# Optimization experiments

Measured on AMD Instinct MI355X. Metric: run time of the kernel, lower is better.

The kernel has to match this reference:

```python
import jax, jax.numpy as jnp
import numpy as np

B, S, D, H = 4, 2048, 1024, 16
NEG = -1e10  # matches the module's -10000000000.0 additive mask


def setup_inputs() -> dict:
    key = jax.random.key(0)
    k1, k2, k3, k4, k5 = jax.random.split(key, 5)
    scale = 0.02
    return {
        "x": jax.random.normal(k1, (B, S, D), dtype=jnp.float32),
        "w_qkv": jax.random.normal(k2, (D, 3 * D), dtype=jnp.float32) * scale,
        "b_qkv": jax.random.normal(k3, (3 * D,), dtype=jnp.float32) * scale,
        "w_out": jax.random.normal(k4, (D, D), dtype=jnp.float32) * scale,
        "b_out": jax.random.normal(k5, (D,), dtype=jnp.float32) * scale,
    }


def reference(x, w_qkv, b_qkv, w_out, b_out):
    b, s, d = x.shape
    hd = d // H  # per-head dim
    qkv = x @ w_qkv + b_qkv  # [b,s,3d]
    qq, kk, vv = jnp.split(qkv, 3, axis=-1)
    # [b,h,s,hd]
    qq = qq.reshape(b, s, H, hd).transpose(0, 2, 1, 3)
    kk = kk.reshape(b, s, H, hd).transpose(0, 2, 1, 3)
    vv = vv.reshape(b, s, H, hd).transpose(0, 2, 1, 3)
    scale = 1.0 / float(hd) ** 0.5
    # additive causal mask: NEG above diagonal, 0 on/below (as in module)
    mask = (1.0 - jnp.tri(s, dtype=jnp.float32)) * NEG
    attn = jnp.einsum("bhqd,bhkd->bhqk", qq, kk) * scale + mask
    attn = jax.nn.softmax(attn, axis=-1)
    out = jnp.einsum("bhqk,bhkd->bhqd", attn, vv)  # [b,h,s,hd]
    out = out.transpose(0, 2, 1, 3).reshape(b, s, d)
    return out @ w_out + b_out
```

## Files before the change

kernel.cpp:

```cpp
#include <hip/hip_runtime.h>
#include <hip/hip_bf16.h>
#include <stdint.h>


#define B_   4
#define S_   2048
#define D_   1024
#define H_   16
#define HD_  64
#define MTOK (B_ * S_)
#define BK   32
#define QSCALE 0.18033688011112042f

typedef __attribute__((ext_vector_type(8))) short bfx8;
typedef __attribute__((ext_vector_type(4))) float fx4;

static __device__ __forceinline__ unsigned short f2bf(float f) {
    union { float f; uint32_t u; } v{f};
    uint32_t u = v.u;
    u += 0x7fffu + ((u >> 16) & 1u);
    return (unsigned short)(u >> 16);
}

static __device__ __forceinline__ uint32_t cvtpk(float lo, float hi) {
    uint32_t r;
    asm volatile("v_cvt_pk_bf16_f32 %0, %1, %2" : "=v"(r) : "v"(lo), "v"(hi));
    return r;
}

static __device__ __forceinline__ void gll16(const unsigned short* g, const unsigned short* l) {
    typedef const __attribute__((address_space(1))) void* gp_t;
    typedef __attribute__((address_space(3))) void* lp_t;
    __builtin_amdgcn_global_load_lds((gp_t)(uintptr_t)g, (lp_t)(uint32_t)(uintptr_t)l, 16, 0, 0);
}

__global__ void k_conv_x(const float* __restrict__ x, unsigned short* __restrict__ xb, int n8) {
    int i = blockIdx.x * blockDim.x + threadIdx.x;
    int stride = gridDim.x * blockDim.x;
    for (; i < n8; i += stride) {
        const float4* p = (const float4*)(x + (size_t)i * 8);
        float4 a = p[0], b = p[1];
        bfx8 o;
        o[0]=f2bf(a.x); o[1]=f2bf(a.y); o[2]=f2bf(a.z); o[3]=f2bf(a.w);
        o[4]=f2bf(b.x); o[5]=f2bf(b.y); o[6]=f2bf(b.z); o[7]=f2bf(b.w);
        *(bfx8*)(xb + (size_t)i * 8) = o;
    }
}

__global__ void k_transpose_bf(const float* __restrict__ w, unsigned short* __restrict__ wt,
                               int K, int N) {
    int idx = blockIdx.x * blockDim.x + threadIdx.x;
    int total = N * (K / 8);
    if (idx >= total) return;
    int n  = idx % N;
    int k0 = (idx / N) * 8;
    bfx8 o;
#pragma unroll
    for (int j = 0; j < 8; ++j) o[j] = f2bf(w[(size_t)(k0 + j) * N + n]);
    *(bfx8*)(wt + (size_t)n * K + k0) = o;
}

__global__ void k_transpose_v(const unsigned short* __restrict__ Vw,
                              unsigned short* __restrict__ Vt) {
    __shared__ unsigned short lds[64][72];
    const int bg = blockIdx.x;
    const int bh = bg >> 5;
    const int st = (bg & 31) * 64;
    const int t = threadIdx.x;
#pragma unroll
    for (int j = 0; j < 2; ++j) {
        int c = t + 256 * j;
        int row = c >> 3, q = c & 7;
        *(bfx8*)&lds[row][q * 8] = *(const bfx8*)&Vw[((size_t)bh * S_ + st + row) * HD_ + q * 8];
    }
    __syncthreads();
#pragma unroll
    for (int j = 0; j < 2; ++j) {
        int c = t + 256 * j;
        int d = c >> 3, q = c & 7;
        bfx8 o;
#pragma unroll
        for (int e = 0; e < 8; ++e) o[e] = lds[q * 8 + e][d];
        *(bfx8*)&Vt[((size_t)bh * HD_ + d) * S_ + st + q * 8] = o;
    }
}

__launch_bounds__(256)
__global__ void k_gemm_qkv(const unsigned short* __restrict__ A,
                           const unsigned short* __restrict__ Bt,
                           const float* __restrict__ bias,
                           unsigned short* __restrict__ Qw,
                           unsigned short* __restrict__ Kw,
                           unsigned short* __restrict__ Vw) {
    __shared__ unsigned short Al[128 * BK];
    __shared__ unsigned short Bl[128 * BK];
    const int wg = blockIdx.x;
    const int lin = (wg & 7) * 192 + (wg >> 3);
    const int ny = lin / 24, nx = lin - ny * 24;
    const int m0 = ny * 128;
    const int n0 = nx * 128;
    const int t = threadIdx.x;
    const int w = t >> 6, l = t & 63;
    const int wr = w >> 1, wc = w & 1;
    const int lr = l & 15, lg = l >> 4;
    const int srow = l >> 2;
    const int scol = (l & 3) * 8;
    fx4 acc[4][4] = {};

    for (int k0 = 0; k0 < D_; k0 += BK) {
        __syncthreads();
#pragma unroll
        for (int j = 0; j < 2; ++j) {
            int rb = j * 64 + w * 16;
            gll16(&A [(size_t)(m0 + rb + srow) * D_ + k0 + scol], &Al[rb * BK]);
            gll16(&Bt[(size_t)(n0 + rb + srow) * D_ + k0 + scol], &Bl[rb * BK]);
        }
        __syncthreads();
        bfx8 af[4], bf[4];
#pragma unroll
        for (int i = 0; i < 4; ++i) af[i] = *(const bfx8*)&Al[(wr * 64 + i * 16 + lr) * BK + lg * 8];
#pragma unroll
        for (int i = 0; i < 4; ++i) bf[i] = *(const bfx8*)&Bl[(wc * 64 + i * 16 + lr) * BK + lg * 8];
#pragma unroll
        for (int mi = 0; mi < 4; ++mi)
#pragma unroll
            for (int ni = 0; ni < 4; ++ni)
                acc[mi][ni] = __builtin_amdgcn_mfma_f32_16x16x32_bf16(bf[ni], af[mi], acc[mi][ni], 0, 0, 0);
    }

#pragma unroll
    for (int ni = 0; ni < 4; ++ni) {
        const int nn = n0 + wc * 64 + ni * 16 + lg * 4;
        const int mat = nn >> 10;
        const int h = (nn & 1023) >> 6, dd = nn & 63;
        const float4 bv = *(const float4*)&bias[nn];
        unsigned short* dst = (mat == 0) ? Qw : (mat == 1) ? Kw : Vw;
        const float sc = (mat == 0) ? QSCALE : 1.0f;
#pragma unroll
        for (int mi = 0; mi < 4; ++mi) {
            const int m = m0 + wr * 64 + mi * 16 + lr;
            const int b = m >> 11, s = m & 2047;
            const int bh = b * H_ + h;
            fx4 v = acc[mi][ni];
            float o0 = (v[0] + bv.x) * sc, o1 = (v[1] + bv.y) * sc;
            float o2 = (v[2] + bv.z) * sc, o3 = (v[3] + bv.w) * sc;
            uint2 u; u.x = cvtpk(o0, o1); u.y = cvtpk(o2, o3);
            *(uint2*)&dst[((size_t)bh * S_ + s) * HD_ + dd] = u;
        }
    }
}

__launch_bounds__(512, 4)
__global__ void k_attn(const unsigned short* __restrict__ Qw,
                       const unsigned short* __restrict__ Kw,
                       const unsigned short* __restrict__ Vt,
                       unsigned short* __restrict__ Ob) {
    __shared__ unsigned short Kl[2][64 * 64];
    __shared__ unsigned short Vl[2][64 * 64];
    __shared__ unsigned short Pl[8][16 * 64];
    const int wg = blockIdx.x;
    const int xcd = wg & 7, ix = wg >> 3;
    const int bh = xcd * 8 + (ix >> 3);
    const int pi = ix & 7;
    const int t = threadIdx.x;
    const int w = t >> 6, l = t & 63;
    const int lr = l & 15, lg = l >> 4;
    const int qA = pi * 128 + w * 16;
    const int qB = (15 - pi) * 128 + w * 16;
    const int NT = 32 - 2 * pi;

    const unsigned short* Qp = Qw + (size_t)bh * S_ * HD_;
    const unsigned short* Kp = Kw + (size_t)bh * S_ * HD_;
    const unsigned short* Vp = Vt + (size_t)bh * HD_ * S_;

    bfx8 qfA[2], qfB[2];
#pragma unroll
    for (int kk = 0; kk < 2; ++kk) {
        qfA[kk] = *(const bfx8*)&Qp[(size_t)(qA + lr) * HD_ + kk * 32 + lg * 8];
        qfB[kk] = *(const bfx8*)&Qp[(size_t)(qB + lr) * HD_ + kk * 32 + lg * 8];
    }

    bfx8 ones;
#pragma unroll
    for (int j = 0; j < 8; ++j) ones[j] = (short)0x3F80;

    fx4 oA[4] = {}, oB[4] = {};
    fx4 sA = {}, sB = {};
    float mA = -1e30f, mB = -1e30f;

    auto compute = [&](int qr, const bfx8* qf, fx4* oacc, fx4& osum, float& mrow,
                       int kv0, int buf) {
        fx4 sacc[4] = {};
        __builtin_amdgcn_s_setprio(1);
#pragma unroll
        for (int c = 0; c < 4; ++c) {
            int row = c * 16 + lr;
#pragma unroll
            for (int kk = 0; kk < 2; ++kk) {
                int colb = kk * 64 + lg * 16;
                bfx8 kf = *(const bfx8*)((const char*)&Kl[buf][0] + row * 128 + (colb ^ ((row & 7) << 4)));
                sacc[c] = __builtin_amdgcn_mfma_f32_16x16x32_bf16(kf, qf[kk], sacc[c], 0, 0, 0);
            }
        }
        __builtin_amdgcn_s_setprio(0);
        if (kv0 + 63 > qr) {
            const int qrel = qr + lr - kv0;
#pragma unroll
            for (int c = 0; c < 4; ++c)
#pragma unroll
                for (int i = 0; i < 4; ++i)
                    if (c * 16 + lg * 4 + i > qrel) sacc[c][i] = -1e30f;
        }
        float mc0 = fmaxf(fmaxf(sacc[0][0], sacc[0][1]), fmaxf(sacc[0][2], sacc[0][3]));
        float mc1 = fmaxf(fmaxf(sacc[1][0], sacc[1][1]), fmaxf(sacc[1][2], sacc[1][3]));
        float mc2 = fmaxf(fmaxf(sacc[2][0], sacc[2][1]), fmaxf(sacc[2][2], sacc[2][3]));
        float mc3 = fmaxf(fmaxf(sacc[3][0], sacc[3][1]), fmaxf(sacc[3][2], sacc[3][3]));
        float mx = fmaxf(fmaxf(mc0, mc1), fmaxf(mc2, mc3));
        mx = fmaxf(mx, __shfl_xor(mx, 16));
        mx = fmaxf(mx, __shfl_xor(mx, 32));
        if (!__all(mx <= mrow + 8.f)) {
            float mnew = fmaxf(mrow, mx);
            float al = exp2f(mrow - mnew);
            mrow = mnew;
#pragma unroll
            for (int c = 0; c < 4; ++c)
#pragma unroll
                for (int i = 0; i < 4; ++i) oacc[c][i] *= al;
            osum[0] *= al;
        }
#pragma unroll
        for (int c = 0; c < 4; ++c) {
            float p0 = exp2f(sacc[c][0] - mrow);
            float p1 = exp2f(sacc[c][1] - mrow);
            float p2 = exp2f(sacc[c][2] - mrow);
            float p3 = exp2f(sacc[c][3] - mrow);
            uint2 u; u.x = cvtpk(p0, p1); u.y = cvtpk(p2, p3);
            *(uint2*)((char*)&Pl[w][0] + lr * 128 + ((c * 32 + lg * 8) ^ ((lr & 7) << 4))) = u;
        }
        __builtin_amdgcn_s_setprio(1);
#pragma unroll
        for (int kk = 0; kk < 2; ++kk) {
            bfx8 pf = *(const bfx8*)((const char*)&Pl[w][0] + lr * 128 + ((kk * 64 + lg * 16) ^ ((lr & 7) << 4)));
            osum = __builtin_amdgcn_mfma_f32_16x16x32_bf16(ones, pf, osum, 0, 0, 0);
#pragma unroll
            for (int c = 0; c < 4; ++c) {
                int vrow = c * 16 + lr;
                int vcolb = kk * 64 + lg * 16;
                bfx8 vf = *(const bfx8*)((const char*)&Vl[buf][0] + vrow * 128 + (vcolb ^ ((vrow & 7) << 4)));
                oacc[c] = __builtin_amdgcn_mfma_f32_16x16x32_bf16(vf, pf, oacc[c], 0, 0, 0);
            }
        }
        __builtin_amdgcn_s_setprio(0);
    };

    {
        bfx8 sreg[2];
#pragma unroll
        for (int it = 0; it < 2; ++it) {
            int id = t + 512 * it;
            int c = id & 511;
            int row = c >> 3, q = c & 7;
            if (id < 512) sreg[it] = *(const bfx8*)&Kp[(size_t)row * HD_ + q * 8];
            else          sreg[it] = *(const bfx8*)&Vp[(size_t)row * S_ + q * 8];
        }
#pragma unroll
        for (int it = 0; it < 2; ++it) {
            int id = t + 512 * it;
            int c = id & 511;
            int row = c >> 3, q = c & 7;
            int off = row * 128 + ((q * 16) ^ ((row & 7) << 4));
            char* base = (id < 512) ? (char*)&Kl[0][0] : (char*)&Vl[0][0];
            *(bfx8*)(base + off) = sreg[it];
        }
    }
    __syncthreads();

    int buf = 0;
    for (int tkv = 0; tkv < NT; ++tkv) {
        const int kv0 = tkv * 64;
        const bool pre = (tkv + 1 < NT);
        bfx8 sreg[2];
        if (pre) {
            const int kn = kv0 + 64;
#pragma unroll
            for (int it = 0; it < 2; ++it) {
                int id = t + 512 * it;
                int c = id & 511;
                int row = c >> 3, q = c & 7;
                if (id < 512) sreg[it] = *(const bfx8*)&Kp[(size_t)(kn + row) * HD_ + q * 8];
                else          sreg[it] = *(const bfx8*)&Vp[(size_t)row * S_ + kn + q * 8];
            }
        }
        if (kv0 <= qB + 15) compute(qB, qfB, oB, sB, mB, kv0, buf);
        if (kv0 <= qA + 15) compute(qA, qfA, oA, sA, mA, kv0, buf);
        if (pre) {
#pragma unroll
            for (int it = 0; it < 2; ++it) {
                int id = t + 512 * it;
                int c = id & 511;
                int row = c >> 3, q = c & 7;
                int off = row * 128 + ((q * 16) ^ ((row & 7) << 4));
                char* base = (id < 512) ? (char*)&Kl[buf ^ 1][0] : (char*)&Vl[buf ^ 1][0];
                *(bfx8*)(base + off) = sreg[it];
            }
        }
        __syncthreads();
        buf ^= 1;
    }

    const int b = bh >> 4, h = bh & 15;
    const float ivA = __builtin_amdgcn_rcpf(sA[0]);
    const float ivB = __builtin_amdgcn_rcpf(sB[0]);
#pragma unroll
    for (int c = 0; c < 4; ++c) {
        uint2 ua, ub;
        ua.x = cvtpk(oA[c][0] * ivA, oA[c][1] * ivA);
        ua.y = cvtpk(oA[c][2] * ivA, oA[c][3] * ivA);
        ub.x = cvtpk(oB[c][0] * ivB, oB[c][1] * ivB);
        ub.y = cvtpk(oB[c][2] * ivB, oB[c][3] * ivB);
        int col = h * 64 + c * 16 + lg * 4;
        *(uint2*)&Ob[((size_t)b * S_ + qA + lr) * D_ + col] = ua;
        *(uint2*)&Ob[((size_t)b * S_ + qB + lr) * D_ + col] = ub;
    }
}

__launch_bounds__(256)
__global__ void k_gemm_proj(const unsigned short* __restrict__ A,
                            const unsigned short* __restrict__ Bt,
                            const float* __restrict__ bias,
                            float* __restrict__ out) {
    __shared__ unsigned short Al[128 * BK];
    __shared__ unsigned short Bl[128 * BK];
    const int wg = blockIdx.x;
    const int lin = (wg & 7) * 64 + (wg >> 3);
    const int ny = lin >> 3, nx = lin & 7;
    const int m0 = ny * 128;
    const int n0 = nx * 128;
    const int t = threadIdx.x;
    const int w = t >> 6, l = t & 63;
    const int wr = w >> 1, wc = w & 1;
    const int lr = l & 15, lg = l >> 4;
    const int srow = l >> 2;
    const int scol = (l & 3) * 8;
    fx4 acc[4][4] = {};

    for (int k0 = 0; k0 < D_; k0 += BK) {
        __syncthreads();
#pragma unroll
        for (int j = 0; j < 2; ++j) {
            int rb = j * 64 + w * 16;
            gll16(&A [(size_t)(m0 + rb + srow) * D_ + k0 + scol], &Al[rb * BK]);
            gll16(&Bt[(size_t)(n0 + rb + srow) * D_ + k0 + scol], &Bl[rb * BK]);
        }
        __syncthreads();
        bfx8 af[4], bf[4];
#pragma unroll
        for (int i = 0; i < 4; ++i) af[i] = *(const bfx8*)&Al[(wr * 64 + i * 16 + lr) * BK + lg * 8];
#pragma unroll
        for (int i = 0; i < 4; ++i) bf[i] = *(const bfx8*)&Bl[(wc * 64 + i * 16 + lr) * BK + lg * 8];
#pragma unroll
        for (int mi = 0; mi < 4; ++mi)
#pragma unroll
            for (int ni = 0; ni < 4; ++ni)
                acc[mi][ni] = __builtin_amdgcn_mfma_f32_16x16x32_bf16(bf[ni], af[mi], acc[mi][ni], 0, 0, 0);
    }
#pragma unroll
    for (int ni = 0; ni < 4; ++ni) {
        const int nn = n0 + wc * 64 + ni * 16 + lg * 4;
        const float4 bv = *(const float4*)&bias[nn];
#pragma unroll
        for (int mi = 0; mi < 4; ++mi) {
            const int m = m0 + wr * 64 + mi * 16 + lr;
            fx4 v = acc[mi][ni];
            float4 o; o.x = v[0] + bv.x; o.y = v[1] + bv.y; o.z = v[2] + bv.z; o.w = v[3] + bv.w;
            *(float4*)&out[(size_t)m * D_ + nn] = o;
        }
    }
}

extern "C" void kernel_launch(void* const* d_in, const int* in_sizes, int n_in,
                              void* d_out, int out_size, void* d_ws, size_t ws_size,
                              hipStream_t stream) {
    const float* x     = (const float*)d_in[0];
    const float* w_qkv = (const float*)d_in[1];
    const float* b_qkv = (const float*)d_in[2];
    const float* w_out = (const float*)d_in[3];
    const float* b_out = (const float*)d_in[4];
    float* out = (float*)d_out;

    unsigned short* xb    = (unsigned short*)d_ws;
    unsigned short* wqkvT = xb    + (size_t)MTOK * D_;
    unsigned short* woutT = wqkvT + (size_t)3 * D_ * D_;
    unsigned short* Qw    = woutT + (size_t)D_ * D_;
    unsigned short* Kw    = Qw    + (size_t)MTOK * D_;
    unsigned short* Vw    = Kw    + (size_t)MTOK * D_;
    unsigned short* attnb = Vw    + (size_t)MTOK * D_;
    unsigned short* Vt    = xb;

    k_conv_x<<<2048, 256, 0, stream>>>(x, xb, MTOK * D_ / 8);
    k_transpose_bf<<<(3 * D_ * (D_ / 8)) / 256, 256, 0, stream>>>(w_qkv, wqkvT, D_, 3 * D_);
    k_transpose_bf<<<(D_ * (D_ / 8)) / 256, 256, 0, stream>>>(w_out, woutT, D_, D_);
    k_gemm_qkv<<<1536, 256, 0, stream>>>(xb, wqkvT, b_qkv, Qw, Kw, Vw);
    k_transpose_v<<<2048, 256, 0, stream>>>(Vw, Vt);
    k_attn<<<512, 512, 0, stream>>>(Qw, Kw, Vt, attnb);
    k_gemm_proj<<<512, 256, 0, stream>>>(attnb, woutT, b_out, out);
}
```

Baseline: 206.9 us.

## Switch attention to 32x32x16 MFMA with register-resident P via permlane swap

```diff
diff --git a/kernel.cpp b/kernel.cpp
--- a/kernel.cpp
+++ b/kernel.cpp
@@ -14,6 +14,7 @@
 
 typedef __attribute__((ext_vector_type(8))) short bfx8;
 typedef __attribute__((ext_vector_type(4))) float fx4;
+typedef __attribute__((ext_vector_type(16))) float fx16;
 
 static __device__ __forceinline__ unsigned short f2bf(float f) {
     union { float f; uint32_t u; } v{f};
@@ -26,6 +27,10 @@
     uint32_t r;
     asm volatile("v_cvt_pk_bf16_f32 %0, %1, %2" : "=v"(r) : "v"(lo), "v"(hi));
     return r;
+}
+
+static __device__ __forceinline__ void pswap(uint32_t& a, uint32_t& b) {
+    asm volatile("v_permlane32_swap_b32 %0, %1" : "+v"(a), "+v"(b));
 }
 
 static __device__ __forceinline__ void gll16(const unsigned short* g, const unsigned short* l) {
@@ -157,100 +162,39 @@
                        unsigned short* __restrict__ Ob) {
     __shared__ unsigned short Kl[2][64 * 64];
     __shared__ unsigned short Vl[2][64 * 64];
-    __shared__ unsigned short Pl[8][16 * 64];
     const int wg = blockIdx.x;
     const int xcd = wg & 7, ix = wg >> 3;
     const int bh = xcd * 8 + (ix >> 3);
     const int pi = ix & 7;
     const int t = threadIdx.x;
     const int w = t >> 6, l = t & 63;
-    const int lr = l & 15, lg = l >> 4;
-    const int qA = pi * 128 + w * 16;
-    const int qB = (15 - pi) * 128 + w * 16;
+    const int lq = l & 31, hi = l >> 5;
+    const int tile = (w < 4) ? (15 - pi) : pi;
+    const int qr = tile * 128 + (w & 3) * 32;
     const int NT = 32 - 2 * pi;
 
     const unsigned short* Qp = Qw + (size_t)bh * S_ * HD_;
     const unsigned short* Kp = Kw + (size_t)bh * S_ * HD_;
     const unsigned short* Vp = Vt + (size_t)bh * HD_ * S_;
 
-    bfx8 qfA[2], qfB[2];
-#pragma unroll
-    for (int kk = 0; kk < 2; ++kk) {
-        qfA[kk] = *(const bfx8*)&Qp[(size_t)(qA + lr) * HD_ + kk * 32 + lg * 8];
-        qfB[kk] = *(const bfx8*)&Qp[(size_t)(qB + lr) * HD_ + kk * 32 + lg * 8];
-    }
-
-    bfx8 ones;
-#pragma unroll
-    for (int j = 0; j < 8; ++j) ones[j] = (short)0x3F80;
-
-    fx4 oA[4] = {}, oB[4] = {};
-    fx4 sA = {}, sB = {};
-    float mA = -1e30f, mB = -1e30f;
-
-    auto compute = [&](int qr, const bfx8* qf, fx4* oacc, fx4& osum, float& mrow,
-                       int kv0, int buf) {
-        fx4 sacc[4] = {};
-        __builtin_amdgcn_s_setprio(1);
-#pragma unroll
-        for (int c = 0; c < 4; ++c) {
-            int row = c * 16 + lr;
-#pragma unroll
-            for (int kk = 0; kk < 2; ++kk) {
-                int colb = kk * 64 + lg * 16;
-                bfx8 kf = *(const bfx8*)((const char*)&Kl[buf][0] + row * 128 + (colb ^ ((row & 7) << 4)));
-                sacc[c] = __builtin_amdgcn_mfma_f32_16x16x32_bf16(kf, qf[kk], sacc[c], 0, 0, 0);
-            }
-        }
-        __builtin_amdgcn_s_setprio(0);
-        if (kv0 + 63 > qr) {
-            const int qrel = qr + lr - kv0;
-#pragma unroll
-            for (int c = 0; c < 4; ++c)
-#pragma unroll
-                for (int i = 0; i < 4; ++i)
-                    if (c * 16 + lg * 4 + i > qrel) sacc[c][i] = -1e30f;
-        }
-        float mc0 = fmaxf(fmaxf(sacc[0][0], sacc[0][1]), fmaxf(sacc[0][2], sacc[0][3]));
-        float mc1 = fmaxf(fmaxf(sacc[1][0], sacc[1][1]), fmaxf(sacc[1][2], sacc[1][3]));
-        float mc2 = fmaxf(fmaxf(sacc[2][0], sacc[2][1]), fmaxf(sacc[2][2], sacc[2][3]));
-        float mc3 = fmaxf(fmaxf(sacc[3][0], sacc[3][1]), fmaxf(sacc[3][2], sacc[3][3]));
-        float mx = fmaxf(fmaxf(mc0, mc1), fmaxf(mc2, mc3));
-        mx = fmaxf(mx, __shfl_xor(mx, 16));
-        mx = fmaxf(mx, __shfl_xor(mx, 32));
-        if (!__all(mx <= mrow + 8.f)) {
-            float mnew = fmaxf(mrow, mx);
-            float al = exp2f(mrow - mnew);
-            mrow = mnew;
-#pragma unroll
-            for (int c = 0; c < 4; ++c)
-#pragma unroll
-                for (int i = 0; i < 4; ++i) oacc[c][i] *= al;
-            osum[0] *= al;
-        }
-#pragma unroll
-        for (int c = 0; c < 4; ++c) {
-            float p0 = exp2f(sacc[c][0] - mrow);
-            float p1 = exp2f(sacc[c][1] - mrow);
-            float p2 = exp2f(sacc[c][2] - mrow);
-            float p3 = exp2f(sacc[c][3] - mrow);
-            uint2 u; u.x = cvtpk(p0, p1); u.y = cvtpk(p2, p3);
-            *(uint2*)((char*)&Pl[w][0] + lr * 128 + ((c * 32 + lg * 8) ^ ((lr & 7) << 4))) = u;
-        }
-        __builtin_amdgcn_s_setprio(1);
-#pragma unroll
-        for (int kk = 0; kk < 2; ++kk) {
-            bfx8 pf = *(const bfx8*)((const char*)&Pl[w][0] + lr * 128 + ((kk * 64 + lg * 16) ^ ((lr & 7) << 4)));
-            osum = __builtin_amdgcn_mfma_f32_16x16x32_bf16(ones, pf, osum, 0, 0, 0);
-#pragma unroll
-            for (int c = 0; c < 4; ++c) {
-                int vrow = c * 16 + lr;
-                int vcolb = kk * 64 + lg * 16;
-                bfx8 vf = *(const bfx8*)((const char*)&Vl[buf][0] + vrow * 128 + (vcolb ^ ((vrow & 7) << 4)));
-                oacc[c] = __builtin_amdgcn_mfma_f32_16x16x32_bf16(vf, pf, oacc[c], 0, 0, 0);
-            }
-        }
-        __builtin_amdgcn_s_setprio(0);
+    bfx8 qf[4];
+#pragma unroll
+    for (int kb = 0; kb < 4; ++kb)
+        qf[kb] = *(const bfx8*)&Qp[(size_t)(qr + lq) * HD_ + kb * 16 + hi * 8];
+
+    fx16 oacc[2] = {};
+    float mrow = -1e30f, lsum = 0.f;
+
+    auto pvstep = [&](const uint32_t* pk, int s, int cb, int buf) {
+        uint32_t w0 = pk[4 * s], w1 = pk[4 * s + 1], w2 = pk[4 * s + 2], w3 = pk[4 * s + 3];
+        pswap(w0, w2);
+        pswap(w1, w3);
+        union { uint32_t u[4]; bfx8 v; } pf;
+        pf.u[0] = w0; pf.u[1] = w1; pf.u[2] = w2; pf.u[3] = w3;
+        bfx8 v0 = *(const bfx8*)((const char*)&Vl[buf][0] + lq * 128 + (cb ^ ((lq & 7) << 4)));
+        bfx8 v1 = *(const bfx8*)((const char*)&Vl[buf][0] + (32 + lq) * 128 + (cb ^ ((lq & 7) << 4)));
+        oacc[0] = __builtin_amdgcn_mfma_f32_32x32x16_bf16(v0, pf.v, oacc[0], 0, 0, 0);
+        oacc[1] = __builtin_amdgcn_mfma_f32_32x32x16_bf16(v1, pf.v, oacc[1], 0, 0, 0);
     };
 
     {
@@ -291,8 +235,57 @@
                 else          sreg[it] = *(const bfx8*)&Vp[(size_t)row * S_ + kn + q * 8];
             }
         }
-        if (kv0 <= qB + 15) compute(qB, qfB, oB, sB, mB, kv0, buf);
-        if (kv0 <= qA + 15) compute(qA, qfA, oA, sA, mA, kv0, buf);
+        if (kv0 <= qr + 31) {
+            fx16 s0 = {}, s1 = {};
+            __builtin_amdgcn_s_setprio(1);
+#pragma unroll
+            for (int kb = 0; kb < 4; ++kb) {
+                const int cb = kb * 32 + hi * 16;
+                bfx8 k0 = *(const bfx8*)((const char*)&Kl[buf][0] + lq * 128 + (cb ^ ((lq & 7) << 4)));
+                bfx8 k1 = *(const bfx8*)((const char*)&Kl[buf][0] + (32 + lq) * 128 + (cb ^ ((lq & 7) << 4)));
+                s0 = __builtin_amdgcn_mfma_f32_32x32x16_bf16(k0, qf[kb], s0, 0, 0, 0);
+                s1 = __builtin_amdgcn_mfma_f32_32x32x16_bf16(k1, qf[kb], s1, 0, 0, 0);
+            }
+            __builtin_amdgcn_s_setprio(0);
+            if (kv0 + 63 > qr) {
+                const int qrel = qr + lq - kv0;
+#pragma unroll
+                for (int r = 0; r < 16; ++r) {
+                    const int kvo = (r & 3) + 8 * (r >> 2) + 4 * hi;
+                    if (kvo > qrel)      s0[r] = -1e30f;
+                    if (kvo + 32 > qrel) s1[r] = -1e30f;
+                }
+            }
+            float mx = fmaxf(s0[0], s1[0]);
+#pragma unroll
+            for (int r = 1; r < 16; ++r) mx = fmaxf(mx, fmaxf(s0[r], s1[r]));
+            mx = fmaxf(mx, __shfl_xor(mx, 32));
+            if (!__all(mx <= mrow + 8.f)) {
+                const float mnew = fmaxf(mrow, mx);
+                const float al = exp2f(mrow - mnew);
+                mrow = mnew;
+#pragma unroll
+                for (int r = 0; r < 16; ++r) { oacc[0][r] *= al; oacc[1][r] *= al; }
+                lsum *= al;
+            }
+            uint32_t pk0[8], pk1[8];
+            float ps = 0.f;
+#pragma unroll
+            for (int j = 0; j < 8; ++j) {
+                float a0 = exp2f(s0[2 * j] - mrow), b0 = exp2f(s0[2 * j + 1] - mrow);
+                float a1 = exp2f(s1[2 * j] - mrow), b1 = exp2f(s1[2 * j + 1] - mrow);
+                ps += (a0 + b0) + (a1 + b1);
+                pk0[j] = cvtpk(a0, b0);
+                pk1[j] = cvtpk(a1, b1);
+            }
+            lsum += ps + __shfl_xor(ps, 32);
+            __builtin_amdgcn_s_setprio(1);
+            pvstep(pk0, 0, 0 * 32 + hi * 16, buf);
+            pvstep(pk0, 1, 1 * 32 + hi * 16, buf);
+            pvstep(pk1, 0, 2 * 32 + hi * 16, buf);
+            pvstep(pk1, 1, 3 * 32 + hi * 16, buf);
+            __builtin_amdgcn_s_setprio(0);
+        }
         if (pre) {
 #pragma unroll
             for (int it = 0; it < 2; ++it) {
@@ -309,19 +302,17 @@
     }
 
     const int b = bh >> 4, h = bh & 15;
-    const float ivA = __builtin_amdgcn_rcpf(sA[0]);
-    const float ivB = __builtin_amdgcn_rcpf(sB[0]);
-#pragma unroll
-    for (int c = 0; c < 4; ++c) {
-        uint2 ua, ub;
-        ua.x = cvtpk(oA[c][0] * ivA, oA[c][1] * ivA);
-        ua.y = cvtpk(oA[c][2] * ivA, oA[c][3] * ivA);
-        ub.x = cvtpk(oB[c][0] * ivB, oB[c][1] * ivB);
-        ub.y = cvtpk(oB[c][2] * ivB, oB[c][3] * ivB);
-        int col = h * 64 + c * 16 + lg * 4;
-        *(uint2*)&Ob[((size_t)b * S_ + qA + lr) * D_ + col] = ua;
-        *(uint2*)&Ob[((size_t)b * S_ + qB + lr) * D_ + col] = ub;
-    }
+    const float iv = __builtin_amdgcn_rcpf(lsum);
+    unsigned short* orow = Ob + ((size_t)b * S_ + qr + lq) * D_ + h * 64;
+#pragma unroll
+    for (int db = 0; db < 2; ++db)
+#pragma unroll
+        for (int rq = 0; rq < 4; ++rq) {
+            uint2 u;
+            u.x = cvtpk(oacc[db][rq * 4 + 0] * iv, oacc[db][rq * 4 + 1] * iv);
+            u.y = cvtpk(oacc[db][rq * 4 + 2] * iv, oacc[db][rq * 4 + 3] * iv);
+            *(uint2*)&orow[db * 32 + rq * 8 + hi * 4] = u;
+        }
 }
 
 __launch_bounds__(256)
```

Result: no change. 204.3 us (-1.2%).
